# Kernel optimization log

Measured on AMD Instinct MI355X. Metric: run time of the kernel, lower is better.

## Reference

```python
import jax, jax.numpy as jnp
import numpy as np

T, B, I_DIM, H_DIM = 256, 64, 1024, 1024


def setup_inputs() -> dict:
    key = jax.random.key(0)
    k_in, k_wx, k_wh = jax.random.split(key, 3)
    # xavier-normal-ish scale for [hidden, input] matrices
    std_x = float(np.sqrt(2.0 / (I_DIM + H_DIM)))
    std_h = float(np.sqrt(2.0 / (H_DIM + H_DIM)))
    return {
        "inputs": jax.random.normal(k_in, (T, B, I_DIM), dtype=jnp.float32),
        "W_x": jax.random.normal(k_wx, (4, H_DIM, I_DIM), dtype=jnp.float32) * std_x,
        "W_h": jax.random.normal(k_wh, (4, H_DIM, H_DIM), dtype=jnp.float32) * std_h,
        "bias": jnp.zeros((4, H_DIM), dtype=jnp.float32),
        "mask_x": jnp.ones((4, H_DIM, I_DIM), dtype=jnp.float32),
        "mask_h": jnp.ones((4, H_DIM, H_DIM), dtype=jnp.float32),
        "H0": jnp.zeros((B, H_DIM), dtype=jnp.float32),
        "C0": jnp.zeros((B, H_DIM), dtype=jnp.float32),
    }


def reference(inputs, W_x, W_h, bias, mask_x, mask_h, H0, C0):
    # masked + transposed weights: (4, in_dim, hidden) so X @ W works
    Wx_t = jnp.transpose(W_x * mask_x, (0, 2, 1))  # (4, I, H)
    Wh_t = jnp.transpose(W_h * mask_h, (0, 2, 1))  # (4, H, H)

    # gate order per original indexing: 0=i, 1=f, 2=o, 3=c
    def step(carry, X):
        H, C = carry
        # fused gate GEMMs: (4, B, H)
        g = (jnp.einsum('bi,gih->gbh', X, Wx_t)
             + jnp.einsum('bh,ghk->gbk', H, Wh_t)
             + bias[:, None, :])
        I_g = jax.nn.sigmoid(g[0])
        F_g = jax.nn.sigmoid(g[1])
        O_g = jax.nn.sigmoid(g[2])
        C_t = jnp.tanh(g[3])
        C_new = F_g * C + I_g * C_t
        H_new = O_g * jnp.tanh(C_new)
        return (H_new, C_new), H_new

    (_, _), outputs = jax.lax.scan(step, (H0, C0), inputs)
    return outputs  # (T, B, H)
```

## Files before the change

kernel.cpp:

```cpp
#include <hip/hip_runtime.h>

typedef __attribute__((ext_vector_type(8))) short short8;
typedef __attribute__((ext_vector_type(4))) float floatx4;

#define T_STEPS 256
#define BATCH   64
#define IDIM    1024
#define HDIM    1024
#define KDIM    (IDIM + HDIM)
#define MB      16
#define HB      16
#define NWG     256
#define NTHR    512
#define A_STRIDE (KDIM + 8)

__device__ __forceinline__ unsigned short f2bf(float f) {
  unsigned u = __float_as_uint(f);
  u += 0x7FFFu + ((u >> 16) & 1u);
  return (unsigned short)(u >> 16);
}

__global__ void prep_weights(const float* __restrict__ Wx, const float* __restrict__ Wh,
                             const float* __restrict__ mx, const float* __restrict__ mh,
                             unsigned short* __restrict__ Wcat) {
  int idx = blockIdx.x * blockDim.x + threadIdx.x;
  const int total = 4 * HDIM * KDIM / 4;
  if (idx >= total) return;
  int k4 = idx & (KDIM / 4 - 1);
  int gh = idx >> 9;
  int k = k4 * 4;
  float4 v, m;
  if (k < IDIM) {
    v = *(const float4*)(Wx + (size_t)gh * IDIM + k);
    m = *(const float4*)(mx + (size_t)gh * IDIM + k);
  } else {
    v = *(const float4*)(Wh + (size_t)gh * HDIM + (k - IDIM));
    m = *(const float4*)(mh + (size_t)gh * HDIM + (k - IDIM));
  }
  ushort4 o;
  o.x = f2bf(v.x * m.x); o.y = f2bf(v.y * m.y);
  o.z = f2bf(v.z * m.z); o.w = f2bf(v.w * m.w);
  *(ushort4*)(Wcat + (size_t)gh * KDIM + k) = o;
}

__global__ void prep_h0(const float* __restrict__ H0, unsigned short* __restrict__ Hbuf0,
                        unsigned* __restrict__ cnt) {
  int i = blockIdx.x * blockDim.x + threadIdx.x;
  if (i < BATCH * HDIM) Hbuf0[i] = f2bf(H0[i]);
  if (i < 16 * 16) cnt[i] = 0u;
}

__global__ void __launch_bounds__(NTHR, 2)
lstm_main(const float* __restrict__ X,
          const float* __restrict__ bias,
          const float* __restrict__ C0,
          const unsigned short* __restrict__ Wcat,
          unsigned short* __restrict__ Hbuf0,
          unsigned short* __restrict__ Hbuf1,
          unsigned* __restrict__ cnt,
          float* __restrict__ out)
{
  __shared__ __align__(16) unsigned short Ash[MB * A_STRIDE];
  __shared__ float parts[2][4][MB][HB + 1];

  const int tid  = threadIdx.x;
  const int wg   = blockIdx.x;
  const int bg   = wg >> 6;
  const int hg   = wg & 63;
  const int b0   = bg * MB;
  const int h0   = hg * HB;

  const int w    = tid >> 6;
  const int lane = tid & 63;
  const int nl   = lane & 15;
  const int quad = lane >> 4;

  short8 Bfr[4][8];
  {
    const short8* wp = (const short8*)Wcat;
#pragma unroll
    for (int g = 0; g < 4; ++g) {
      const int rowbase = (g * HDIM + h0 + nl) * (KDIM / 8);
#pragma unroll
      for (int ks = 0; ks < 8; ++ks)
        Bfr[g][ks] = wp[rowbase + w * 32 + ks * 4 + quad];
    }
  }

  float c_state = 0.f;
  const int eb = tid >> 4;
  const int eh = tid & 15;
  if (tid < 256) c_state = C0[(b0 + eb) * HDIM + h0 + eh];

  const int e0 = tid, e1 = tid + NTHR;
  const int p0 = (e0 >> 8) * (MB * (HB + 1)) + ((e0 >> 4) & 15) * (HB + 1) + (e0 & 15);
  const int p1 = (e1 >> 8) * (MB * (HB + 1)) + ((e1 >> 4) & 15) * (HB + 1) + (e1 & 15);
  const float binit0 = bias[(e0 >> 8) * HDIM + h0 + (e0 & 15)];
  const float binit1 = bias[(e1 >> 8) * HDIM + h0 + (e1 & 15)];

  const int c8 = tid & 127;
  const int mrow = tid >> 7;

  unsigned* mycnt  = cnt + (bg * 4 + (hg & 3)) * 16;
  unsigned* bgcnt  = cnt + bg * 4 * 16;

  float4 Xpre[8];
  {
    const float4* xp = (const float4*)(X + (size_t)b0 * IDIM);
#pragma unroll
    for (int it = 0; it < 8; ++it) {
      int v = it * NTHR + tid;
      Xpre[it] = xp[(v >> 8) * (IDIM / 4) + (v & 255)];
    }
  }

  for (int t = 0; t < T_STEPS; ++t) {
    const unsigned short* __restrict__ Hprev = (t & 1) ? Hbuf1 : Hbuf0;
    unsigned short* __restrict__ Hnext       = (t & 1) ? Hbuf0 : Hbuf1;
    float* pcur = &parts[t & 1][0][0][0];

#pragma unroll
    for (int it = 0; it < 8; ++it) {
      int v = it * NTHR + tid;
      int m = v >> 8, c4 = v & 255;
      float4 f = Xpre[it];
      ushort4 o;
      o.x = f2bf(f.x); o.y = f2bf(f.y); o.z = f2bf(f.z); o.w = f2bf(f.w);
      *(ushort4*)&Ash[m * A_STRIDE + c4 * 4] = o;
    }
    pcur[p0] = binit0;
    pcur[p1] = binit1;

    if (tid == 0 && t > 0) {
      const unsigned tgt = (unsigned)(64 * t);
      for (;;) {
        unsigned s = __hip_atomic_load(bgcnt +  0, __ATOMIC_RELAXED, __HIP_MEMORY_SCOPE_AGENT)
                   + __hip_atomic_load(bgcnt + 16, __ATOMIC_RELAXED, __HIP_MEMORY_SCOPE_AGENT)
                   + __hip_atomic_load(bgcnt + 32, __ATOMIC_RELAXED, __HIP_MEMORY_SCOPE_AGENT)
                   + __hip_atomic_load(bgcnt + 48, __ATOMIC_RELAXED, __HIP_MEMORY_SCOPE_AGENT);
        if (s >= tgt) break;
        __builtin_amdgcn_s_sleep(8);
      }
    }
    __syncthreads();

    {
      const unsigned short* pa = Hprev + (size_t)(b0 + mrow) * HDIM + c8 * 8;
      uint4 d0, d1, d2, d3;
      asm volatile(
        "global_load_dwordx4 %0, %4, off sc0 sc1\n\t"
        "global_load_dwordx4 %1, %5, off sc0 sc1\n\t"
        "global_load_dwordx4 %2, %6, off sc0 sc1\n\t"
        "global_load_dwordx4 %3, %7, off sc0 sc1\n\t"
        "s_waitcnt vmcnt(0)"
        : "=&v"(d0), "=&v"(d1), "=&v"(d2), "=&v"(d3)
        : "v"(pa), "v"(pa + 4 * HDIM), "v"(pa + 8 * HDIM), "v"(pa + 12 * HDIM)
        : "memory");
      *(uint4*)&Ash[(mrow +  0) * A_STRIDE + IDIM + c8 * 8] = d0;
      *(uint4*)&Ash[(mrow +  4) * A_STRIDE + IDIM + c8 * 8] = d1;
      *(uint4*)&Ash[(mrow +  8) * A_STRIDE + IDIM + c8 * 8] = d2;
      *(uint4*)&Ash[(mrow + 12) * A_STRIDE + IDIM + c8 * 8] = d3;
    }
    __syncthreads();

    {
      int tn = (t + 1 < T_STEPS) ? t + 1 : t;
      const float4* xp = (const float4*)(X + ((size_t)tn * BATCH + b0) * IDIM);
#pragma unroll
      for (int it = 0; it < 8; ++it) {
        int v = it * NTHR + tid;
        Xpre[it] = xp[(v >> 8) * (IDIM / 4) + (v & 255)];
      }
    }

    floatx4 acc[4];
#pragma unroll
    for (int g = 0; g < 4; ++g) acc[g] = floatx4{0.f, 0.f, 0.f, 0.f};
    {
      const unsigned short* abase = &Ash[nl * A_STRIDE + w * 256 + quad * 8];
#pragma unroll
      for (int ks = 0; ks < 8; ++ks) {
        short8 af = *(const short8*)(abase + ks * 32);
#pragma unroll
        for (int g = 0; g < 4; ++g)
          acc[g] = __builtin_amdgcn_mfma_f32_16x16x32_bf16(af, Bfr[g][ks], acc[g], 0, 0, 0);
      }
    }
#pragma unroll
    for (int g = 0; g < 4; ++g)
#pragma unroll
      for (int r = 0; r < 4; ++r)
        atomicAdd(&parts[t & 1][g][quad * 4 + r][nl], acc[g][r]);
    __syncthreads();

    if (tid < 256) {
      float gI = parts[t & 1][0][eb][eh];
      float gF = parts[t & 1][1][eb][eh];
      float gO = parts[t & 1][2][eb][eh];
      float gC = parts[t & 1][3][eb][eh];
      float ig = 1.f / (1.f + __expf(-gI));
      float fg = 1.f / (1.f + __expf(-gF));
      float og = 1.f / (1.f + __expf(-gO));
      float cb = 1.f - 2.f / (__expf(2.f * gC) + 1.f);
      c_state = fg * c_state + ig * cb;
      float hn = og * (1.f - 2.f / (__expf(2.f * c_state) + 1.f));
      unsigned short hb = f2bf(hn);
      unsigned short* ps = Hnext + (size_t)(b0 + eb) * HDIM + h0 + eh;
      asm volatile("global_store_short %0, %1, off sc0 sc1"
                   :: "v"(ps), "v"((unsigned)hb) : "memory");
      out[((size_t)t * BATCH + b0 + eb) * HDIM + h0 + eh] = hn;
    }
    asm volatile("s_waitcnt vmcnt(0)" ::: "memory");
    __syncthreads();
    if (tid == 0) atomicAdd(mycnt, 1u);
  }
}

extern "C" void kernel_launch(void* const* d_in, const int* in_sizes, int n_in,
                              void* d_out, int out_size, void* d_ws, size_t ws_size,
                              hipStream_t stream) {
  const float* X    = (const float*)d_in[0];
  const float* Wx   = (const float*)d_in[1];
  const float* Wh   = (const float*)d_in[2];
  const float* bias = (const float*)d_in[3];
  const float* mx   = (const float*)d_in[4];
  const float* mh   = (const float*)d_in[5];
  const float* H0   = (const float*)d_in[6];
  const float* C0   = (const float*)d_in[7];
  float* out = (float*)d_out;

  unsigned short* Wcat  = (unsigned short*)d_ws;
  unsigned short* Hbuf0 = Wcat + (size_t)4 * HDIM * KDIM;
  unsigned short* Hbuf1 = Hbuf0 + BATCH * HDIM;
  unsigned*       cnt   = (unsigned*)(Hbuf1 + BATCH * HDIM);

  {
    int tot = 4 * HDIM * KDIM / 4;
    prep_weights<<<(tot + 255) / 256, 256, 0, stream>>>(Wx, Wh, mx, mh, Wcat);
  }
  prep_h0<<<(BATCH * HDIM + 255) / 256, 256, 0, stream>>>(H0, Hbuf0, cnt);

  void* args[] = { (void*)&X, (void*)&bias, (void*)&C0, (void*)&Wcat,
                   (void*)&Hbuf0, (void*)&Hbuf1, (void*)&cnt, (void*)&out };
  hipLaunchCooperativeKernel(reinterpret_cast<void*>(lstm_main),
                             dim3(NWG), dim3(NTHR), args, 0, stream);
}
```

Measured before the change: 3.475 ms.

## Overlap input GEMM with barrier wait, use per-tile flags and tiled H layout

Splits the per-step GEMM into an input part (X·Wx), computed before waiting on other workgroups, and a recurrent part (H·Wh) computed after the wait. This takes the input projection off the serial critical path. The shared counters with atomic sums are replaced by one monotonic flag per workgroup, polled in parallel by 64 lanes with a shorter sleep. H is stored in a tiled layout so each workgroup writes one contiguous 16x16 tile. The output store is moved after the flag publish. The cost is more atomic adds to shared memory per step and more polling traffic.

```diff
diff --git a/kernel.cpp b/kernel.cpp
--- a/kernel.cpp
+++ b/kernel.cpp
@@ -43,11 +43,15 @@
   *(ushort4*)(Wcat + (size_t)gh * KDIM + k) = o;
 }
 
-__global__ void prep_h0(const float* __restrict__ H0, unsigned short* __restrict__ Hbuf0,
-                        unsigned* __restrict__ cnt) {
+__global__ void prep_htile(const float* __restrict__ H0, unsigned short* __restrict__ Htile,
+                           unsigned* __restrict__ flags) {
   int i = blockIdx.x * blockDim.x + threadIdx.x;
-  if (i < BATCH * HDIM) Hbuf0[i] = f2bf(H0[i]);
-  if (i < 16 * 16) cnt[i] = 0u;
+  if (i < BATCH * HDIM) {
+    int b = i >> 10, h = i & 1023;
+    int bg = b >> 4, r = b & 15, hg = h >> 4, c = h & 15;
+    Htile[((bg * 64 + hg) * 256) + r * 16 + c] = f2bf(H0[i]);
+  }
+  if (i < 4 * 64 * 16) flags[i] = 0u;
 }
 
 __global__ void __launch_bounds__(NTHR, 2)
@@ -55,9 +59,8 @@
           const float* __restrict__ bias,
           const float* __restrict__ C0,
           const unsigned short* __restrict__ Wcat,
-          unsigned short* __restrict__ Hbuf0,
-          unsigned short* __restrict__ Hbuf1,
-          unsigned* __restrict__ cnt,
+          unsigned short* __restrict__ Htile,
+          unsigned* __restrict__ flags,
           float* __restrict__ out)
 {
   __shared__ __align__(16) unsigned short Ash[MB * A_STRIDE];
@@ -75,15 +78,17 @@
   const int nl   = lane & 15;
   const int quad = lane >> 4;
 
-  short8 Bfr[4][8];
+  short8 BfrX[4][4], BfrH[4][4];
   {
     const short8* wp = (const short8*)Wcat;
 #pragma unroll
     for (int g = 0; g < 4; ++g) {
       const int rowbase = (g * HDIM + h0 + nl) * (KDIM / 8);
 #pragma unroll
-      for (int ks = 0; ks < 8; ++ks)
-        Bfr[g][ks] = wp[rowbase + w * 32 + ks * 4 + quad];
+      for (int ks = 0; ks < 4; ++ks) {
+        BfrX[g][ks] = wp[rowbase + w * 16 + ks * 4 + quad];
+        BfrH[g][ks] = wp[rowbase + 128 + w * 16 + ks * 4 + quad];
+      }
     }
   }
 
@@ -98,11 +103,13 @@
   const float binit0 = bias[(e0 >> 8) * HDIM + h0 + (e0 & 15)];
   const float binit1 = bias[(e1 >> 8) * HDIM + h0 + (e1 & 15)];
 
-  const int c8 = tid & 127;
+  const int c8   = tid & 127;
   const int mrow = tid >> 7;
-
-  unsigned* mycnt  = cnt + (bg * 4 + (hg & 3)) * 16;
-  unsigned* bgcnt  = cnt + bg * 4 * 16;
+  const int hgp  = c8 >> 1;
+  const int cin  = (c8 & 1) * 8;
+
+  unsigned* myflag  = flags + (bg * 64 + hg) * 16;
+  const unsigned* lflag = flags + (bg * 64 + lane) * 16;
 
   float4 Xpre[8];
   {
@@ -115,8 +122,6 @@
   }
 
   for (int t = 0; t < T_STEPS; ++t) {
-    const unsigned short* __restrict__ Hprev = (t & 1) ? Hbuf1 : Hbuf0;
-    unsigned short* __restrict__ Hnext       = (t & 1) ? Hbuf0 : Hbuf1;
     float* pcur = &parts[t & 1][0][0][0];
 
 #pragma unroll
@@ -130,22 +135,52 @@
     }
     pcur[p0] = binit0;
     pcur[p1] = binit1;
-
-    if (tid == 0 && t > 0) {
-      const unsigned tgt = (unsigned)(64 * t);
+    __syncthreads();
+
+    {
+      floatx4 accx[4];
+#pragma unroll
+      for (int g = 0; g < 4; ++g) accx[g] = floatx4{0.f, 0.f, 0.f, 0.f};
+      const unsigned short* abase = &Ash[nl * A_STRIDE + w * 128 + quad * 8];
+#pragma unroll
+      for (int ks = 0; ks < 4; ++ks) {
+        short8 af = *(const short8*)(abase + ks * 32);
+#pragma unroll
+        for (int g = 0; g < 4; ++g)
+          accx[g] = __builtin_amdgcn_mfma_f32_16x16x32_bf16(af, BfrX[g][ks], accx[g], 0, 0, 0);
+      }
+#pragma unroll
+      for (int g = 0; g < 4; ++g)
+#pragma unroll
+        for (int r = 0; r < 4; ++r)
+          atomicAdd(&parts[t & 1][g][quad * 4 + r][nl], accx[g][r]);
+    }
+    {
+      int tn = (t + 1 < T_STEPS) ? t + 1 : t;
+      const float4* xp = (const float4*)(X + ((size_t)tn * BATCH + b0) * IDIM);
+#pragma unroll
+      for (int it = 0; it < 8; ++it) {
+        int v = it * NTHR + tid;
+        Xpre[it] = xp[(v >> 8) * (IDIM / 4) + (v & 255)];
+      }
+    }
+
+    if (t > 0 && tid < 64) {
+      const unsigned tgt = (unsigned)t;
       for (;;) {
-        unsigned s = __hip_atomic_load(bgcnt +  0, __ATOMIC_RELAXED, __HIP_MEMORY_SCOPE_AGENT)
-                   + __hip_atomic_load(bgcnt + 16, __ATOMIC_RELAXED, __HIP_MEMORY_SCOPE_AGENT)
-                   + __hip_atomic_load(bgcnt + 32, __ATOMIC_RELAXED, __HIP_MEMORY_SCOPE_AGENT)
-                   + __hip_atomic_load(bgcnt + 48, __ATOMIC_RELAXED, __HIP_MEMORY_SCOPE_AGENT);
-        if (s >= tgt) break;
-        __builtin_amdgcn_s_sleep(8);
-      }
-    }
-    __syncthreads();
-
-    {
-      const unsigned short* pa = Hprev + (size_t)(b0 + mrow) * HDIM + c8 * 8;
+        unsigned v;
+        asm volatile("global_load_dword %0, %1, off sc0 sc1\n\t"
+                     "s_waitcnt vmcnt(0)"
+                     : "=v"(v) : "v"(lflag) : "memory");
+        if (v >= tgt) break;
+        __builtin_amdgcn_s_sleep(1);
+      }
+    }
+    __syncthreads();
+
+    {
+      const unsigned short* tb = Htile + ((size_t)(t & 1) * 4 + bg) * (64 * 256);
+      const unsigned short* pa = tb + hgp * 256 + mrow * 16 + cin;
       uint4 d0, d1, d2, d3;
       asm volatile(
         "global_load_dwordx4 %0, %4, off sc0 sc1\n\t"
@@ -154,7 +189,7 @@
         "global_load_dwordx4 %3, %7, off sc0 sc1\n\t"
         "s_waitcnt vmcnt(0)"
         : "=&v"(d0), "=&v"(d1), "=&v"(d2), "=&v"(d3)
-        : "v"(pa), "v"(pa + 4 * HDIM), "v"(pa + 8 * HDIM), "v"(pa + 12 * HDIM)
+        : "v"(pa), "v"(pa + 64), "v"(pa + 128), "v"(pa + 192)
         : "memory");
       *(uint4*)&Ash[(mrow +  0) * A_STRIDE + IDIM + c8 * 8] = d0;
       *(uint4*)&Ash[(mrow +  4) * A_STRIDE + IDIM + c8 * 8] = d1;
@@ -164,35 +199,26 @@
     __syncthreads();
 
     {
-      int tn = (t + 1 < T_STEPS) ? t + 1 : t;
-      const float4* xp = (const float4*)(X + ((size_t)tn * BATCH + b0) * IDIM);
-#pragma unroll
-      for (int it = 0; it < 8; ++it) {
-        int v = it * NTHR + tid;
-        Xpre[it] = xp[(v >> 8) * (IDIM / 4) + (v & 255)];
-      }
-    }
-
-    floatx4 acc[4];
-#pragma unroll
-    for (int g = 0; g < 4; ++g) acc[g] = floatx4{0.f, 0.f, 0.f, 0.f};
-    {
-      const unsigned short* abase = &Ash[nl * A_STRIDE + w * 256 + quad * 8];
-#pragma unroll
-      for (int ks = 0; ks < 8; ++ks) {
+      floatx4 acch[4];
+#pragma unroll
+      for (int g = 0; g < 4; ++g) acch[g] = floatx4{0.f, 0.f, 0.f, 0.f};
+      const unsigned short* abase = &Ash[nl * A_STRIDE + IDIM + w * 128 + quad * 8];
+#pragma unroll
+      for (int ks = 0; ks < 4; ++ks) {
         short8 af = *(const short8*)(abase + ks * 32);
 #pragma unroll
         for (int g = 0; g < 4; ++g)
-          acc[g] = __builtin_amdgcn_mfma_f32_16x16x32_bf16(af, Bfr[g][ks], acc[g], 0, 0, 0);
-      }
-    }
-#pragma unroll
-    for (int g = 0; g < 4; ++g)
-#pragma unroll
-      for (int r = 0; r < 4; ++r)
-        atomicAdd(&parts[t & 1][g][quad * 4 + r][nl], acc[g][r]);
-    __syncthreads();
-
+          acch[g] = __builtin_amdgcn_mfma_f32_16x16x32_bf16(af, BfrH[g][ks], acch[g], 0, 0, 0);
+      }
+#pragma unroll
+      for (int g = 0; g < 4; ++g)
+#pragma unroll
+        for (int r = 0; r < 4; ++r)
+          atomicAdd(&parts[t & 1][g][quad * 4 + r][nl], acch[g][r]);
+    }
+    __syncthreads();
+
+    float hn = 0.f;
     if (tid < 256) {
       float gI = parts[t & 1][0][eb][eh];
       float gF = parts[t & 1][1][eb][eh];
@@ -203,16 +229,22 @@
       float og = 1.f / (1.f + __expf(-gO));
       float cb = 1.f - 2.f / (__expf(2.f * gC) + 1.f);
       c_state = fg * c_state + ig * cb;
-      float hn = og * (1.f - 2.f / (__expf(2.f * c_state) + 1.f));
+      hn = og * (1.f - 2.f / (__expf(2.f * c_state) + 1.f));
       unsigned short hb = f2bf(hn);
-      unsigned short* ps = Hnext + (size_t)(b0 + eb) * HDIM + h0 + eh;
+      unsigned short* nb = Htile + ((size_t)((t + 1) & 1) * 4 + bg) * (64 * 256)
+                         + hg * 256 + tid;
       asm volatile("global_store_short %0, %1, off sc0 sc1"
-                   :: "v"(ps), "v"((unsigned)hb) : "memory");
+                   :: "v"(nb), "v"((unsigned)hb) : "memory");
+    }
+    asm volatile("s_waitcnt vmcnt(0)" ::: "memory");
+    __syncthreads();
+    if (tid == 0) {
+      unsigned fv = (unsigned)(t + 1);
+      asm volatile("global_store_dword %0, %1, off sc0 sc1"
+                   :: "v"(myflag), "v"(fv) : "memory");
+    }
+    if (tid < 256)
       out[((size_t)t * BATCH + b0 + eb) * HDIM + h0 + eh] = hn;
-    }
-    asm volatile("s_waitcnt vmcnt(0)" ::: "memory");
-    __syncthreads();
-    if (tid == 0) atomicAdd(mycnt, 1u);
   }
 }
 
@@ -230,18 +262,17 @@
   float* out = (float*)d_out;
 
   unsigned short* Wcat  = (unsigned short*)d_ws;
-  unsigned short* Hbuf0 = Wcat + (size_t)4 * HDIM * KDIM;
-  unsigned short* Hbuf1 = Hbuf0 + BATCH * HDIM;
-  unsigned*       cnt   = (unsigned*)(Hbuf1 + BATCH * HDIM);
+  unsigned short* Htile = Wcat + (size_t)4 * HDIM * KDIM;
+  unsigned*       flags = (unsigned*)(Htile + 2 * 4 * 64 * 256);
 
   {
     int tot = 4 * HDIM * KDIM / 4;
     prep_weights<<<(tot + 255) / 256, 256, 0, stream>>>(Wx, Wh, mx, mh, Wcat);
   }
-  prep_h0<<<(BATCH * HDIM + 255) / 256, 256, 0, stream>>>(H0, Hbuf0, cnt);
+  prep_htile<<<(BATCH * HDIM + 255) / 256, 256, 0, stream>>>(H0, Htile, flags);
 
   void* args[] = { (void*)&X, (void*)&bias, (void*)&C0, (void*)&Wcat,
-                   (void*)&Hbuf0, (void*)&Hbuf1, (void*)&cnt, (void*)&out };
+                   (void*)&Htile, (void*)&flags, (void*)&out };
   hipLaunchCooperativeKernel(reinterpret_cast<void*>(lstm_main),
                              dim3(NWG), dim3(NTHR), args, 0, stream);
 }
```

Measured after the change: 6.155 ms. +77.1%, slower.
